# Performance work log

Hardware: AMD Instinct MI355X
Metric: run time of the kernel (lower is better)

Reference implementation:

```python
import jax, jax.numpy as jnp
import numpy as np

B, T, C, H = 2, 2048, 1024, 16
DH = C // H  # 64


def setup_inputs() -> dict:
    key = jax.random.key(0)
    ks = jax.random.split(key, 8)
    scale = 1.0 / np.sqrt(C)
    x = jax.random.normal(ks[0], (B, T, C), dtype=jnp.float32)
    mask = jax.random.randint(ks[1], (B, T), 0, 2, dtype=jnp.int32)
    Wq = jax.random.normal(ks[2], (C, C), dtype=jnp.float32) * scale
    bq = jnp.zeros((C,), dtype=jnp.float32)
    Wk = jax.random.normal(ks[3], (C, C), dtype=jnp.float32) * scale
    bk = jnp.zeros((C,), dtype=jnp.float32)
    Wv = jax.random.normal(ks[4], (C, C), dtype=jnp.float32) * scale
    bv = jnp.zeros((C,), dtype=jnp.float32)
    return {"x": x, "Wq": Wq, "bq": bq, "Wk": Wk, "bk": bk, "Wv": Wv, "bv": bv, "mask": mask}


def reference(x, Wq, bq, Wk, bk, Wv, bv, mask):
    # q/k/v projections: [B,T,C] -> [B,H,T,DH]
    def proj(W, b):
        return (x @ W + b).reshape(B, T, H, DH).transpose(0, 2, 1, 3)

    q = proj(Wq, bq)
    k = proj(Wk, bk)
    v = proj(Wv, bv)

    att = jnp.einsum("bhqd,bhkd->bhqk", q, k) * (1.0 / np.sqrt(DH))

    # outer-product padding mask: square_mask[b,q,k] = mask[b,q]*mask[b,k]
    m = mask.astype(jnp.float32)
    square_mask = m[:, :, None] * m[:, None, :]           # [B,T,T]
    sm = (square_mask != 0)[:, None, :, :]                 # [B,1,T,T]
    att = jnp.where(sm, att, -jnp.inf)

    # rows that are fully masked (query token padded) -> softmax gives NaN
    # in torch; torch then zeros the NaNs. Replicate with a safe softmax.
    row_valid = (mask != 0)[:, None, :, None]              # [B,1,T,1]
    att_safe = jnp.where(row_valid, att, 0.0)
    att = jax.nn.softmax(att_safe, axis=-1)
    att = jnp.where(row_valid, att, 0.0)
    # attn_pdrop = 0.0 -> dropout is identity

    y = jnp.einsum("bhqk,bhkd->bhqd", att, v)              # [B,H,T,DH]
    y = y.transpose(0, 2, 1, 3).reshape(B, T, C)
    return y
```

## Files before the change

kernel.cpp:

```cpp
#include <hip/hip_runtime.h>

#define B_ 2
#define T_ 2048
#define C_ 1024
#define H_ 16
#define DH_ 64

typedef __attribute__((ext_vector_type(8))) _Float16 half8;
typedef __attribute__((ext_vector_type(4))) _Float16 half4;
typedef __attribute__((ext_vector_type(2))) __fp16 fp16x2;
typedef __attribute__((ext_vector_type(4))) float f32x4;

__device__ __forceinline__ unsigned short f2h(float f) {
    union { _Float16 h; unsigned short u; } cv; cv.h = (_Float16)f; return cv.u;
}
__device__ __forceinline__ unsigned pk2(float a, float b) {
    union { fp16x2 h; unsigned u; } cv;
    cv.h = __builtin_amdgcn_cvt_pkrtz(a, b);
    return cv.u;
}

__device__ __forceinline__ void gll16(const void* g, void* l) {
    __builtin_amdgcn_global_load_lds(
        (const __attribute__((address_space(1))) void*)g,
        (__attribute__((address_space(3))) void*)l, 16, 0, 0);
}

__global__ __launch_bounds__(256) void prep_kernel(
    const float* __restrict__ x, unsigned short* __restrict__ xf,
    const int* __restrict__ mask, unsigned short* __restrict__ mb,
    const float* __restrict__ Wq, const float* __restrict__ Wk,
    const float* __restrict__ Wv, unsigned short* __restrict__ wt)
{
    __shared__ float tile[32][33];
    const int tid = threadIdx.x;

    if (blockIdx.x < 2048) {
        const size_t idx8 = ((size_t)blockIdx.x * 256 + tid) * 8;
        float4 v0 = *(const float4*)(x + idx8);
        float4 v1 = *(const float4*)(x + idx8 + 4);
        float f[8] = {v0.x, v0.y, v0.z, v0.w, v1.x, v1.y, v1.z, v1.w};
        unsigned short h[8];
#pragma unroll
        for (int i = 0; i < 8; i++) h[i] = f2h(f[i]);
        *(uint4*)(xf + idx8) = *(const uint4*)h;

        if (blockIdx.x == 0) {
#pragma unroll
            for (int j = 0; j < 16; j++) {
                int i = tid * 16 + j;
                mb[i] = (mask[i] != 0) ? (unsigned short)0x3C00 : (unsigned short)0;
            }
        }
    } else {
        const int idx = blockIdx.x - 2048;
        const int z   = idx >> 10;
        const int rem = idx & 1023;
        const int n0  = (rem & 31) * 32;
        const int k0  = (rem >> 5) * 32;
        const float* __restrict__ W = (z == 0) ? Wq : (z == 1) ? Wk : Wv;
        unsigned short* __restrict__ wtz = wt + (size_t)z * C_ * C_;
        const int tx = tid & 31;
        const int ty = tid >> 5;
#pragma unroll
        for (int j = 0; j < 4; j++)
            tile[ty + j * 8][tx] = W[(size_t)(k0 + ty + j * 8) * C_ + n0 + tx];
        __syncthreads();
#pragma unroll
        for (int j = 0; j < 4; j++)
            wtz[(size_t)(n0 + ty + j * 8) * C_ + k0 + tx] = f2h(tile[tx][ty + j * 8]);
    }
}

__global__ __launch_bounds__(256) void qkv_mfma_kernel(
    const unsigned short* __restrict__ xf, const unsigned short* __restrict__ wt,
    const float* __restrict__ bq, const float* __restrict__ bk,
    const float* __restrict__ bv, const int* __restrict__ maskp,
    unsigned short* __restrict__ qb, unsigned short* __restrict__ kb,
    unsigned short* __restrict__ vt)
{
    __shared__ unsigned short sX[128 * 64];
    __shared__ unsigned short sW[128 * 64];

    const int z = blockIdx.z;
    const float* __restrict__ bias = (z == 0) ? bq : (z == 1) ? bk : bv;
    const unsigned short* __restrict__ wtz = wt + (size_t)z * C_ * C_;

    const int tok0 = blockIdx.x * 128;
    const int col0 = blockIdx.y * 128;
    const int wv    = threadIdx.x >> 6;
    const int lane  = threadIdx.x & 63;
    const int l15   = lane & 15;
    const int quad  = lane >> 4;
    const int l7    = l15 & 7;
    const int wm    = wv >> 1;
    const int wn    = wv & 1;
    const int lrow8 = lane >> 3;
    const int gch   = (lane & 7) ^ lrow8;

    f32x4 acc[4][4];
#pragma unroll
    for (int i = 0; i < 4; i++)
#pragma unroll
        for (int j = 0; j < 4; j++) acc[i][j] = (f32x4){0.f, 0.f, 0.f, 0.f};

    int aoff[4][2], boff[4][2];
#pragma unroll
    for (int i = 0; i < 4; i++)
#pragma unroll
        for (int s = 0; s < 2; s++) {
            aoff[i][s] = (wm * 64 + i * 16 + l15) * 64 + (((s * 4 + quad) ^ l7) * 8);
            boff[i][s] = (wn * 64 + i * 16 + l15) * 64 + (((s * 4 + quad) ^ l7) * 8);
        }

    const unsigned short* Abuf = (z < 2) ? sX : sW;
    const unsigned short* Bbuf = (z < 2) ? sW : sX;

    for (int k0 = 0; k0 < C_; k0 += 64) {
        __syncthreads();
#pragma unroll
        for (int s = 0; s < 8; ++s) {
            int g    = (s << 2) + wv;
            int tsel = g >> 4;
            int r0   = (g & 15) << 3;
            const unsigned short* src = tsel ? wtz : xf;
            unsigned short*       dst = tsel ? sW  : sX;
            int rowg = tsel ? col0 : tok0;
            gll16(src + (size_t)(rowg + r0 + lrow8) * C_ + k0 + gch * 8,
                  dst + r0 * 64);
        }
        __syncthreads();

        half8 af[4][2], bf_[4][2];
#pragma unroll
        for (int i = 0; i < 4; i++)
#pragma unroll
            for (int s = 0; s < 2; s++) {
                af[i][s]  = *(const half8*)&Abuf[aoff[i][s]];
                bf_[i][s] = *(const half8*)&Bbuf[boff[i][s]];
            }
#pragma unroll
        for (int s = 0; s < 2; s++)
#pragma unroll
            for (int j = 0; j < 4; j++)
#pragma unroll
                for (int i = 0; i < 4; i++)
                    acc[i][j] = __builtin_amdgcn_mfma_f32_16x16x32_f16(
                        af[i][s], bf_[j][s], acc[i][j], 0, 0, 0);
    }

    if (z == 0) {
#pragma unroll
        for (int j = 0; j < 4; j++) {
            int col = col0 + wn * 64 + j * 16 + l15;
            int h = col >> 6, d = col & 63;
            float bs = bias[col];
#pragma unroll
            for (int i = 0; i < 4; i++) {
#pragma unroll
                for (int r = 0; r < 4; r++) {
                    int tok = tok0 + wm * 64 + i * 16 + quad * 4 + r;
                    int bidx = tok >> 11, t = tok & (T_ - 1);
                    qb[((size_t)(bidx * H_ + h) * T_ + t) * DH_ + d] =
                        f2h((acc[i][j][r] + bs) * 0.18033688011112042f);
                }
            }
        }
    } else if (z == 1) {
#pragma unroll
        for (int j = 0; j < 4; j++) {
            int col = col0 + wn * 64 + j * 16 + l15;
            int h = col >> 6, d = col & 63;
            float bs = bias[col];
#pragma unroll
            for (int i = 0; i < 4; i++) {
#pragma unroll
                for (int r = 0; r < 4; r++) {
                    int tok = tok0 + wm * 64 + i * 16 + quad * 4 + r;
                    int bidx = tok >> 11, t = tok & (T_ - 1);
                    kb[((size_t)(bidx * H_ + h) * T_ + t) * DH_ + d] =
                        f2h(acc[i][j][r] + bs);
                }
            }
        }
    } else {
        float mv4[4]; int bidx4[4], t4[4];
#pragma unroll
        for (int j = 0; j < 4; j++) {
            int tok = tok0 + wn * 64 + j * 16 + l15;
            bidx4[j] = tok >> 11; t4[j] = tok & (T_ - 1);
            mv4[j] = (maskp[bidx4[j] * T_ + t4[j]] != 0) ? 1.f : 0.f;
        }
#pragma unroll
        for (int i = 0; i < 4; i++) {
#pragma unroll
            for (int r = 0; r < 4; r++) {
                int col = col0 + wm * 64 + i * 16 + quad * 4 + r;
                int h = col >> 6, d = col & 63;
                float bs = bias[col];
#pragma unroll
                for (int j = 0; j < 4; j++) {
                    vt[((size_t)(bidx4[j] * H_ + h) * DH_ + d) * T_ + t4[j]] =
                        f2h((acc[i][j][r] + bs) * mv4[j]);
                }
            }
        }
    }
}

__global__ __launch_bounds__(256) void attn_mfma_kernel(
    const unsigned short* __restrict__ qb,
    const unsigned short* __restrict__ kb,
    const unsigned short* __restrict__ vt,
    const int* __restrict__ mask,
    const unsigned short* __restrict__ mb,
    float* __restrict__ out)
{
    __shared__ unsigned short Ks[2][64 * 64];
    __shared__ unsigned short Vs[2][64 * 64];

    const int bh   = blockIdx.x;
    const int b    = bh >> 4;
    const int h    = bh & 15;
    const int wv   = threadIdx.x >> 6;
    const int lane = threadIdx.x & 63;
    const int l15  = lane & 15;
    const int quad = lane >> 4;
    const int l7   = l15 & 7;
    const int q0w  = blockIdx.y * 128 + wv * 32;

    const unsigned short* kbh = kb + (size_t)bh * T_ * DH_;
    const unsigned short* vbh = vt + (size_t)bh * DH_ * T_;
    const unsigned short* mbb = mb + b * T_;
    const int* __restrict__ mrow = mask + b * T_;

    half8 qf[2][2];
#pragma unroll
    for (int qt = 0; qt < 2; ++qt)
#pragma unroll
        for (int c = 0; c < 2; ++c)
            qf[qt][c] = *(const half8*)(qb + ((size_t)bh * T_ + q0w + qt * 16 + l15) * DH_
                                        + c * 32 + quad * 8);

    f32x4 o[2][4];
#pragma unroll
    for (int qt = 0; qt < 2; ++qt)
#pragma unroll
        for (int n = 0; n < 4; ++n) o[qt][n] = (f32x4){0.f, 0.f, 0.f, 0.f};
    f32x4 lacc[2];
    lacc[0] = (f32x4){0.f, 0.f, 0.f, 0.f};
    lacc[1] = (f32x4){0.f, 0.f, 0.f, 0.f};

    const int lrow = lane >> 3;
    const int gch  = (lane & 7) ^ lrow;

#pragma unroll
    for (int s = 0; s < 4; ++s) {
        int j  = (wv << 2) + s;
        int rb = j & 7;
        if (j < 8) gll16(kbh + (size_t)(rb * 8 + lrow) * DH_ + gch * 8, &Ks[0][rb * 512]);
        else       gll16(vbh + (size_t)(rb * 8 + lrow) * T_  + gch * 8, &Vs[0][rb * 512]);
    }

    for (int kt = 0; kt < 32; ++kt) {
        const int cur   = kt & 1;
        const int kbase = kt * 64;
        __syncthreads();

        if (kt < 31) {
            const int nb = kbase + 64;
#pragma unroll
            for (int s = 0; s < 4; ++s) {
                int j  = (wv << 2) + s;
                int rb = j & 7;
                if (j < 8) gll16(kbh + (size_t)(nb + rb * 8 + lrow) * DH_ + gch * 8,
                                 &Ks[cur ^ 1][rb * 512]);
                else       gll16(vbh + (size_t)(rb * 8 + lrow) * T_ + nb + gch * 8,
                                 &Vs[cur ^ 1][rb * 512]);
            }
        }

        const unsigned short* Kc = &Ks[cur][0];
        const unsigned short* Vc = &Vs[cur][0];

        half8 kf[4][2];
#pragma unroll
        for (int ktile = 0; ktile < 4; ++ktile)
#pragma unroll
            for (int c = 0; c < 2; ++c)
                kf[ktile][c] = *(const half8*)(Kc + (ktile * 16 + l15) * 64
                                               + (((c * 4 + quad) ^ l7) * 8));

        half4 vb[4][4];
#pragma unroll
        for (int n = 0; n < 4; ++n)
#pragma unroll
            for (int ktile = 0; ktile < 4; ++ktile)
                vb[n][ktile] = *(const half4*)(Vc + (n * 16 + l15) * 64
                                               + (((ktile * 2 + (quad >> 1)) ^ l7) * 8)
                                               + (quad & 1) * 4);

        half4 bmf[4];
#pragma unroll
        for (int ktile = 0; ktile < 4; ++ktile) {
            half4 mv = *(const half4*)(mbb + kbase + ktile * 16 + quad * 4);
            bmf[ktile] = (l15 == 0) ? mv : (half4)0;
        }

#pragma unroll
        for (int qt = 0; qt < 2; ++qt) {
            half4 pa[4];
#pragma unroll
            for (int ktile = 0; ktile < 4; ++ktile) {
                f32x4 st = (f32x4){0.f, 0.f, 0.f, 0.f};
                st = __builtin_amdgcn_mfma_f32_16x16x32_f16(kf[ktile][0], qf[qt][0], st, 0, 0, 0);
                st = __builtin_amdgcn_mfma_f32_16x16x32_f16(kf[ktile][1], qf[qt][1], st, 0, 0, 0);
                union { uint2 u; half4 h; } cv;
                cv.u.x = pk2(__builtin_amdgcn_exp2f(st[0]), __builtin_amdgcn_exp2f(st[1]));
                cv.u.y = pk2(__builtin_amdgcn_exp2f(st[2]), __builtin_amdgcn_exp2f(st[3]));
                pa[ktile] = cv.h;
            }

#pragma unroll
            for (int ktile = 0; ktile < 4; ++ktile)
                lacc[qt] = __builtin_amdgcn_mfma_f32_16x16x16f16(
                    pa[ktile], bmf[ktile], lacc[qt], 0, 0, 0);

#pragma unroll
            for (int n = 0; n < 4; ++n)
#pragma unroll
                for (int ktile = 0; ktile < 4; ++ktile)
                    o[qt][n] = __builtin_amdgcn_mfma_f32_16x16x16f16(
                        pa[ktile], vb[n][ktile], o[qt][n], 0, 0, 0);
        }
    }

#pragma unroll
    for (int qt = 0; qt < 2; ++qt) {
#pragma unroll
        for (int r = 0; r < 4; ++r) {
            float lv = __shfl(lacc[qt][r], quad << 4, 64);
            int q = q0w + qt * 16 + quad * 4 + r;
            float iv = (mrow[q] != 0 && lv > 0.f) ? (1.0f / lv) : 0.f;
            float* orow = out + ((size_t)(b * T_ + q)) * C_ + h * DH_;
#pragma unroll
            for (int n = 0; n < 4; ++n)
                orow[n * 16 + l15] = o[qt][n][r] * iv;
        }
    }
}

extern "C" void kernel_launch(void* const* d_in, const int* in_sizes, int n_in,
                              void* d_out, int out_size, void* d_ws, size_t ws_size,
                              hipStream_t stream)
{
    (void)in_sizes; (void)n_in; (void)out_size; (void)ws_size;
    const float* x  = (const float*)d_in[0];
    const float* Wq = (const float*)d_in[1];
    const float* bq = (const float*)d_in[2];
    const float* Wk = (const float*)d_in[3];
    const float* bk = (const float*)d_in[4];
    const float* Wv = (const float*)d_in[5];
    const float* bv = (const float*)d_in[6];
    const int* mask = (const int*)d_in[7];
    float* out = (float*)d_out;

    const size_t NX = (size_t)B_ * T_ * C_;
    unsigned short* xf = (unsigned short*)d_ws;
    unsigned short* wt = xf + NX;
    unsigned short* qb = wt + (size_t)3 * C_ * C_;
    unsigned short* kb = qb + NX;
    unsigned short* vt = kb + NX;
    unsigned short* mb = vt + NX;

    prep_kernel<<<5120, 256, 0, stream>>>(x, xf, mask, mb, Wq, Wk, Wv, wt);
    qkv_mfma_kernel<<<dim3(32, 8, 3), 256, 0, stream>>>(
        xf, wt, bq, bk, bv, mask, qb, kb, vt);
    attn_mfma_kernel<<<dim3(32, 16), 256, 0, stream>>>(qb, kb, vt, mask, mb, out);
}
```

Measured before the change: 167.7 us.

## Split attention block across 8 waves with one 16-row query tile each

The attention kernel now launches 512 threads per block, and each of the 8 waves handles 16 query rows instead of 32. The K/V tile loads are spread over 8 waves, two 16-byte loads per lane. This halves per-wave accumulator and Q registers and doubles the waves available to hide latency. In exchange, each wave reads the shared K/V fragments for half as much MFMA work, which doubles LDS fragment traffic per FLOP.

```diff
diff --git a/kernel.cpp b/kernel.cpp
--- a/kernel.cpp
+++ b/kernel.cpp
@@ -208,7 +208,7 @@
     }
 }
 
-__global__ __launch_bounds__(256) void attn_mfma_kernel(
+__global__ __launch_bounds__(512) void attn_mfma_kernel(
     const unsigned short* __restrict__ qb,
     const unsigned short* __restrict__ kb,
     const unsigned short* __restrict__ vt,
@@ -227,36 +227,30 @@
     const int l15  = lane & 15;
     const int quad = lane >> 4;
     const int l7   = l15 & 7;
-    const int q0w  = blockIdx.y * 128 + wv * 32;
+    const int q0w  = blockIdx.y * 128 + wv * 16;
 
     const unsigned short* kbh = kb + (size_t)bh * T_ * DH_;
     const unsigned short* vbh = vt + (size_t)bh * DH_ * T_;
     const unsigned short* mbb = mb + b * T_;
     const int* __restrict__ mrow = mask + b * T_;
 
-    half8 qf[2][2];
-#pragma unroll
-    for (int qt = 0; qt < 2; ++qt)
-#pragma unroll
-        for (int c = 0; c < 2; ++c)
-            qf[qt][c] = *(const half8*)(qb + ((size_t)bh * T_ + q0w + qt * 16 + l15) * DH_
-                                        + c * 32 + quad * 8);
-
-    f32x4 o[2][4];
-#pragma unroll
-    for (int qt = 0; qt < 2; ++qt)
-#pragma unroll
-        for (int n = 0; n < 4; ++n) o[qt][n] = (f32x4){0.f, 0.f, 0.f, 0.f};
-    f32x4 lacc[2];
-    lacc[0] = (f32x4){0.f, 0.f, 0.f, 0.f};
-    lacc[1] = (f32x4){0.f, 0.f, 0.f, 0.f};
+    half8 qf[2];
+#pragma unroll
+    for (int c = 0; c < 2; ++c)
+        qf[c] = *(const half8*)(qb + ((size_t)bh * T_ + q0w + l15) * DH_
+                                + c * 32 + quad * 8);
+
+    f32x4 o[4];
+#pragma unroll
+    for (int n = 0; n < 4; ++n) o[n] = (f32x4){0.f, 0.f, 0.f, 0.f};
+    f32x4 lacc = (f32x4){0.f, 0.f, 0.f, 0.f};
 
     const int lrow = lane >> 3;
     const int gch  = (lane & 7) ^ lrow;
 
 #pragma unroll
-    for (int s = 0; s < 4; ++s) {
-        int j  = (wv << 2) + s;
+    for (int s = 0; s < 2; ++s) {
+        int j  = (wv << 1) + s;
         int rb = j & 7;
         if (j < 8) gll16(kbh + (size_t)(rb * 8 + lrow) * DH_ + gch * 8, &Ks[0][rb * 512]);
         else       gll16(vbh + (size_t)(rb * 8 + lrow) * T_  + gch * 8, &Vs[0][rb * 512]);
@@ -270,8 +264,8 @@
         if (kt < 31) {
             const int nb = kbase + 64;
 #pragma unroll
-            for (int s = 0; s < 4; ++s) {
-                int j  = (wv << 2) + s;
+            for (int s = 0; s < 2; ++s) {
+                int j  = (wv << 1) + s;
                 int rb = j & 7;
                 if (j < 8) gll16(kbh + (size_t)(nb + rb * 8 + lrow) * DH_ + gch * 8,
                                  &Ks[cur ^ 1][rb * 512]);
@@ -307,46 +301,40 @@
             bmf[ktile] = (l15 == 0) ? mv : (half4)0;
         }
 
-#pragma unroll
-        for (int qt = 0; qt < 2; ++qt) {
-            half4 pa[4];
-#pragma unroll
-            for (int ktile = 0; ktile < 4; ++ktile) {
-                f32x4 st = (f32x4){0.f, 0.f, 0.f, 0.f};
-                st = __builtin_amdgcn_mfma_f32_16x16x32_f16(kf[ktile][0], qf[qt][0], st, 0, 0, 0);
-                st = __builtin_amdgcn_mfma_f32_16x16x32_f16(kf[ktile][1], qf[qt][1], st, 0, 0, 0);
-                union { uint2 u; half4 h; } cv;
-                cv.u.x = pk2(__builtin_amdgcn_exp2f(st[0]), __builtin_amdgcn_exp2f(st[1]));
-                cv.u.y = pk2(__builtin_amdgcn_exp2f(st[2]), __builtin_amdgcn_exp2f(st[3]));
-                pa[ktile] = cv.h;
-            }
-
+        half4 pa[4];
+#pragma unroll
+        for (int ktile = 0; ktile < 4; ++ktile) {
+            f32x4 st = (f32x4){0.f, 0.f, 0.f, 0.f};
+            st = __builtin_amdgcn_mfma_f32_16x16x32_f16(kf[ktile][0], qf[0], st, 0, 0, 0);
+            st = __builtin_amdgcn_mfma_f32_16x16x32_f16(kf[ktile][1], qf[1], st, 0, 0, 0);
+            union { uint2 u; half4 h; } cv;
+            cv.u.x = pk2(__builtin_amdgcn_exp2f(st[0]), __builtin_amdgcn_exp2f(st[1]));
+            cv.u.y = pk2(__builtin_amdgcn_exp2f(st[2]), __builtin_amdgcn_exp2f(st[3]));
+            pa[ktile] = cv.h;
+        }
+
+#pragma unroll
+        for (int ktile = 0; ktile < 4; ++ktile)
+            lacc = __builtin_amdgcn_mfma_f32_16x16x16f16(
+                pa[ktile], bmf[ktile], lacc, 0, 0, 0);
+
+#pragma unroll
+        for (int n = 0; n < 4; ++n)
 #pragma unroll
             for (int ktile = 0; ktile < 4; ++ktile)
-                lacc[qt] = __builtin_amdgcn_mfma_f32_16x16x16f16(
-                    pa[ktile], bmf[ktile], lacc[qt], 0, 0, 0);
-
-#pragma unroll
-            for (int n = 0; n < 4; ++n)
-#pragma unroll
-                for (int ktile = 0; ktile < 4; ++ktile)
-                    o[qt][n] = __builtin_amdgcn_mfma_f32_16x16x16f16(
-                        pa[ktile], vb[n][ktile], o[qt][n], 0, 0, 0);
-        }
-    }
-
-#pragma unroll
-    for (int qt = 0; qt < 2; ++qt) {
-#pragma unroll
-        for (int r = 0; r < 4; ++r) {
-            float lv = __shfl(lacc[qt][r], quad << 4, 64);
-            int q = q0w + qt * 16 + quad * 4 + r;
-            float iv = (mrow[q] != 0 && lv > 0.f) ? (1.0f / lv) : 0.f;
-            float* orow = out + ((size_t)(b * T_ + q)) * C_ + h * DH_;
-#pragma unroll
-            for (int n = 0; n < 4; ++n)
-                orow[n * 16 + l15] = o[qt][n][r] * iv;
-        }
+                o[n] = __builtin_amdgcn_mfma_f32_16x16x16f16(
+                    pa[ktile], vb[n][ktile], o[n], 0, 0, 0);
+    }
+
+#pragma unroll
+    for (int r = 0; r < 4; ++r) {
+        float lv = __shfl(lacc[r], quad << 4, 64);
+        int q = q0w + quad * 4 + r;
+        float iv = (mrow[q] != 0 && lv > 0.f) ? (1.0f / lv) : 0.f;
+        float* orow = out + ((size_t)(b * T_ + q)) * C_ + h * DH_;
+#pragma unroll
+        for (int n = 0; n < 4; ++n)
+            orow[n * 16 + l15] = o[n][r] * iv;
     }
 }
 
@@ -376,5 +364,5 @@
     prep_kernel<<<5120, 256, 0, stream>>>(x, xf, mask, mb, Wq, Wk, Wv, wt);
     qkv_mfma_kernel<<<dim3(32, 8, 3), 256, 0, stream>>>(
         xf, wt, bq, bk, bv, mask, qb, kb, vt);
-    attn_mfma_kernel<<<dim3(32, 16), 256, 0, stream>>>(qb, kb, vt, mask, mb, out);
-}
+    attn_mfma_kernel<<<dim3(32, 16), 512, 0, stream>>>(qb, kb, vt, mask, mb, out);
+}
```

Measured after the change: 173.5 us. 3.5% more time.

## Switch attention inner loop to 32x32x16 MFMA with permlane swap for P operand

Applied to the files above, without the earlier changes.

Rewrites the attention kernel's per-tile compute to use 32x32x16 f16 MFMA instructions instead of 16x16 variants. The S tile is transposed into the A-operand layout for the PV and row-sum products with v_permlane32_swap, and the row sum is broadcast via the mask vector in all columns, so the final shuffle goes away. Launch bounds now request 2 blocks per CU. The aim is fewer MFMA issues, fewer LDS fragment loads and better matrix-core throughput, at the cost of larger 16-wide accumulators and register pressure.

```diff
diff --git a/kernel.cpp b/kernel.cpp
--- a/kernel.cpp
+++ b/kernel.cpp
@@ -10,6 +10,7 @@
 typedef __attribute__((ext_vector_type(4))) _Float16 half4;
 typedef __attribute__((ext_vector_type(2))) __fp16 fp16x2;
 typedef __attribute__((ext_vector_type(4))) float f32x4;
+typedef __attribute__((ext_vector_type(16))) float f32x16;
 
 __device__ __forceinline__ unsigned short f2h(float f) {
     union { _Float16 h; unsigned short u; } cv; cv.h = (_Float16)f; return cv.u;
@@ -18,6 +19,9 @@
     union { fp16x2 h; unsigned u; } cv;
     cv.h = __builtin_amdgcn_cvt_pkrtz(a, b);
     return cv.u;
+}
+__device__ __forceinline__ void plswap(unsigned &a, unsigned &b) {
+    asm volatile("v_permlane32_swap_b32 %0, %1" : "+v"(a), "+v"(b));
 }
 
 __device__ __forceinline__ void gll16(const void* g, void* l) {
@@ -208,7 +212,7 @@
     }
 }
 
-__global__ __launch_bounds__(256) void attn_mfma_kernel(
+__global__ __launch_bounds__(256, 2) void attn_mfma_kernel(
     const unsigned short* __restrict__ qb,
     const unsigned short* __restrict__ kb,
     const unsigned short* __restrict__ vt,
@@ -224,9 +228,9 @@
     const int h    = bh & 15;
     const int wv   = threadIdx.x >> 6;
     const int lane = threadIdx.x & 63;
-    const int l15  = lane & 15;
-    const int quad = lane >> 4;
-    const int l7   = l15 & 7;
+    const int l31  = lane & 31;
+    const int hi   = lane >> 5;
+    const int l7b  = l31 & 7;
     const int q0w  = blockIdx.y * 128 + wv * 32;
 
     const unsigned short* kbh = kb + (size_t)bh * T_ * DH_;
@@ -234,22 +238,15 @@
     const unsigned short* mbb = mb + b * T_;
     const int* __restrict__ mrow = mask + b * T_;
 
-    half8 qf[2][2];
-#pragma unroll
-    for (int qt = 0; qt < 2; ++qt)
-#pragma unroll
-        for (int c = 0; c < 2; ++c)
-            qf[qt][c] = *(const half8*)(qb + ((size_t)bh * T_ + q0w + qt * 16 + l15) * DH_
-                                        + c * 32 + quad * 8);
-
-    f32x4 o[2][4];
-#pragma unroll
-    for (int qt = 0; qt < 2; ++qt)
-#pragma unroll
-        for (int n = 0; n < 4; ++n) o[qt][n] = (f32x4){0.f, 0.f, 0.f, 0.f};
-    f32x4 lacc[2];
-    lacc[0] = (f32x4){0.f, 0.f, 0.f, 0.f};
-    lacc[1] = (f32x4){0.f, 0.f, 0.f, 0.f};
+    half8 qf[4];
+#pragma unroll
+    for (int m = 0; m < 4; ++m)
+        qf[m] = *(const half8*)(qb + ((size_t)bh * T_ + q0w + l31) * DH_
+                                + m * 16 + hi * 8);
+
+    f32x16 o0, o1, lacc;
+#pragma unroll
+    for (int r = 0; r < 16; ++r) { o0[r] = 0.f; o1[r] = 0.f; lacc[r] = 0.f; }
 
     const int lrow = lane >> 3;
     const int gch  = (lane & 7) ^ lrow;
@@ -283,70 +280,61 @@
         const unsigned short* Kc = &Ks[cur][0];
         const unsigned short* Vc = &Vs[cur][0];
 
-        half8 kf[4][2];
-#pragma unroll
-        for (int ktile = 0; ktile < 4; ++ktile)
-#pragma unroll
-            for (int c = 0; c < 2; ++c)
-                kf[ktile][c] = *(const half8*)(Kc + (ktile * 16 + l15) * 64
-                                               + (((c * 4 + quad) ^ l7) * 8));
-
-        half4 vb[4][4];
-#pragma unroll
-        for (int n = 0; n < 4; ++n)
-#pragma unroll
-            for (int ktile = 0; ktile < 4; ++ktile)
-                vb[n][ktile] = *(const half4*)(Vc + (n * 16 + l15) * 64
-                                               + (((ktile * 2 + (quad >> 1)) ^ l7) * 8)
-                                               + (quad & 1) * 4);
-
-        half4 bmf[4];
-#pragma unroll
-        for (int ktile = 0; ktile < 4; ++ktile) {
-            half4 mv = *(const half4*)(mbb + kbase + ktile * 16 + quad * 4);
-            bmf[ktile] = (l15 == 0) ? mv : (half4)0;
-        }
-
-#pragma unroll
-        for (int qt = 0; qt < 2; ++qt) {
-            half4 pa[4];
-#pragma unroll
-            for (int ktile = 0; ktile < 4; ++ktile) {
-                f32x4 st = (f32x4){0.f, 0.f, 0.f, 0.f};
-                st = __builtin_amdgcn_mfma_f32_16x16x32_f16(kf[ktile][0], qf[qt][0], st, 0, 0, 0);
-                st = __builtin_amdgcn_mfma_f32_16x16x32_f16(kf[ktile][1], qf[qt][1], st, 0, 0, 0);
-                union { uint2 u; half4 h; } cv;
-                cv.u.x = pk2(__builtin_amdgcn_exp2f(st[0]), __builtin_amdgcn_exp2f(st[1]));
-                cv.u.y = pk2(__builtin_amdgcn_exp2f(st[2]), __builtin_amdgcn_exp2f(st[3]));
-                pa[ktile] = cv.h;
-            }
-
-#pragma unroll
-            for (int ktile = 0; ktile < 4; ++ktile)
-                lacc[qt] = __builtin_amdgcn_mfma_f32_16x16x16f16(
-                    pa[ktile], bmf[ktile], lacc[qt], 0, 0, 0);
-
-#pragma unroll
-            for (int n = 0; n < 4; ++n)
-#pragma unroll
-                for (int ktile = 0; ktile < 4; ++ktile)
-                    o[qt][n] = __builtin_amdgcn_mfma_f32_16x16x16f16(
-                        pa[ktile], vb[n][ktile], o[qt][n], 0, 0, 0);
-        }
-    }
-
-#pragma unroll
-    for (int qt = 0; qt < 2; ++qt) {
-#pragma unroll
-        for (int r = 0; r < 4; ++r) {
-            float lv = __shfl(lacc[qt][r], quad << 4, 64);
-            int q = q0w + qt * 16 + quad * 4 + r;
-            float iv = (mrow[q] != 0 && lv > 0.f) ? (1.0f / lv) : 0.f;
-            float* orow = out + ((size_t)(b * T_ + q)) * C_ + h * DH_;
-#pragma unroll
-            for (int n = 0; n < 4; ++n)
-                orow[n * 16 + l15] = o[qt][n][r] * iv;
-        }
+        half8 bm[4];
+#pragma unroll
+        for (int c = 0; c < 4; ++c)
+            bm[c] = *(const half8*)(mbb + kbase + c * 16 + hi * 8);
+
+        half8 pa[4];
+#pragma unroll
+        for (int st = 0; st < 2; ++st) {
+            f32x16 sa;
+#pragma unroll
+            for (int r = 0; r < 16; ++r) sa[r] = 0.f;
+#pragma unroll
+            for (int m = 0; m < 4; ++m) {
+                half8 kf = *(const half8*)(Kc + (st * 32 + l31) * 64
+                                           + (((m * 2 + hi) ^ l7b) * 8));
+                sa = __builtin_amdgcn_mfma_f32_32x32x16_f16(kf, qf[m], sa, 0, 0, 0);
+            }
+            float p[16];
+#pragma unroll
+            for (int r = 0; r < 16; ++r) p[r] = __builtin_amdgcn_exp2f(sa[r]);
+#pragma unroll
+            for (int kh = 0; kh < 2; ++kh) {
+                unsigned w0 = pk2(p[kh * 8 + 0], p[kh * 8 + 1]);
+                unsigned w2 = pk2(p[kh * 8 + 4], p[kh * 8 + 5]);
+                unsigned w1 = pk2(p[kh * 8 + 2], p[kh * 8 + 3]);
+                unsigned w3 = pk2(p[kh * 8 + 6], p[kh * 8 + 7]);
+                plswap(w0, w2);
+                plswap(w1, w3);
+                union { unsigned u[4]; half8 hh; } cv;
+                cv.u[0] = w0; cv.u[1] = w1; cv.u[2] = w2; cv.u[3] = w3;
+                pa[st * 2 + kh] = cv.hh;
+            }
+        }
+
+#pragma unroll
+        for (int c = 0; c < 4; ++c)
+            lacc = __builtin_amdgcn_mfma_f32_32x32x16_f16(pa[c], bm[c], lacc, 0, 0, 0);
+
+#pragma unroll
+        for (int c = 0; c < 4; ++c) {
+            half8 v0 = *(const half8*)(Vc + (l31) * 64      + (((c * 2 + hi) ^ l7b) * 8));
+            half8 v1 = *(const half8*)(Vc + (32 + l31) * 64 + (((c * 2 + hi) ^ l7b) * 8));
+            o0 = __builtin_amdgcn_mfma_f32_32x32x16_f16(pa[c], v0, o0, 0, 0, 0);
+            o1 = __builtin_amdgcn_mfma_f32_32x32x16_f16(pa[c], v1, o1, 0, 0, 0);
+        }
+    }
+
+#pragma unroll
+    for (int r = 0; r < 16; ++r) {
+        int q = q0w + (r & 3) + 8 * (r >> 2) + 4 * hi;
+        float lv = lacc[r];
+        float iv = (mrow[q] != 0 && lv > 0.f) ? (1.0f / lv) : 0.f;
+        float* orow = out + ((size_t)(b * T_ + q)) * C_ + h * DH_;
+        orow[l31]      = o0[r] * iv;
+        orow[32 + l31] = o1[r] * iv;
     }
 }
 
```

New measurement: 167.2 us. Within noise of the previous version (-0.2%).
